# Performance work log

Measured on AMD Instinct MI355X. Metric: run time of the kernel, lower is better.

The kernel has to match this reference:

```python
import jax, jax.numpy as jnp
import numpy as np

N_NODES = 65536
N_EDGES = 524288
N_GRAPHS = 512
G_NODES = 10000
NUM_DISEASES = 2000
IN_DIM = 128
HID = 256  # 2 * IN_DIM (z_emb concat feat)
D_FEAT = 512
C_FEAT = 512
MAX_Z = 4000


def setup_inputs() -> dict:
    key = jax.random.key(0)
    ks = jax.random.split(key, 20)
    rn = lambda k, shape: jax.random.normal(k, shape, dtype=jnp.float32) * 0.05
    return {
        "z": jax.random.randint(ks[0], (N_NODES,), 0, MAX_Z),
        "node_id": jnp.sort(jax.random.randint(ks[1], (N_NODES,), 0, G_NODES)),
        "src": jax.random.randint(ks[2], (N_EDGES,), 0, N_NODES),
        "dst": jax.random.randint(ks[3], (N_EDGES,), 0, N_NODES),
        "graph_ids": jnp.sort(jax.random.randint(ks[4], (N_NODES,), 0, N_GRAPHS)),
        "z_table": rn(ks[5], (MAX_Z, IN_DIM)),
        "d_feat_tab": rn(ks[6], (G_NODES, D_FEAT)),
        "c_feat_tab": rn(ks[7], (G_NODES, C_FEAT)),
        "Wd": rn(ks[8], (D_FEAT, IN_DIM)),
        "Wc": rn(ks[9], (C_FEAT, IN_DIM)),
        "gin_W1": rn(ks[10], (HID, HID)), "gin_b1": jnp.zeros((HID,), jnp.float32),
        "gin_W2": rn(ks[11], (HID, HID)), "gin_b2": jnp.zeros((HID,), jnp.float32),
        "sage_Wself": rn(ks[12], (HID, HID)),
        "sage_Wneigh": rn(ks[13], (HID, HID)),
        "sage_b": jnp.zeros((HID,), jnp.float32),
        "lin1_W": rn(ks[14], (HID, HID)), "lin1_b": jnp.zeros((HID,), jnp.float32),
        "lin2_W": rn(ks[15], (HID, 1)), "lin2_b": jnp.zeros((1,), jnp.float32),
    }


def reference(z, node_id, src, dst, graph_ids, z_table, d_feat_tab, c_feat_tab,
              Wd, Wc, gin_W1, gin_b1, gin_W2, gin_b2,
              sage_Wself, sage_Wneigh, sage_b, lin1_W, lin1_b, lin2_W, lin2_b):
    # --- input feature construction (Model.forward) ---
    z_emb = z_table[z]                               # [N, IN_DIM]
    d_proj = d_feat_tab[node_id] @ Wd                # d_fc (bias=False)
    c_proj = c_feat_tab[node_id] @ Wc                # c_fc (bias=False)
    disease = (node_id <= NUM_DISEASES)[:, None]
    # node_id is sorted -> masked concat order == node order
    feat = jnp.where(disease, d_proj, c_proj)        # [N, IN_DIM]
    x = jnp.concatenate([z_emb, feat], axis=1)       # [N, HID]
    # --- GINConv: sum aggregation, eps=0, mlp = Lin->ReLU->Lin ---
    agg = jax.ops.segment_sum(x[src], dst, num_segments=N_NODES)
    h = x + agg
    h = jax.nn.relu(h @ gin_W1 + gin_b1) @ gin_W2 + gin_b2
    # --- SAGEConv('mean'): fc_self(h) + fc_neigh(mean_neighbors) + bias ---
    deg = jax.ops.segment_sum(jnp.ones((N_EDGES,), h.dtype), dst, num_segments=N_NODES)
    mean_n = jax.ops.segment_sum(h[src], dst, num_segments=N_NODES) / jnp.maximum(deg, 1.0)[:, None]
    h = h @ sage_Wself + mean_n @ sage_Wneigh + sage_b
    # --- per-graph max pooling readout ---
    g = jax.ops.segment_max(h, graph_ids, num_segments=N_GRAPHS, indices_are_sorted=True)
    g = jnp.where(jnp.isfinite(g), g, 0.0)           # guard empty graphs
    # --- head: Linear -> ReLU -> (dropout p=0, eval) -> Linear ---
    h = jax.nn.relu(g @ lin1_W + lin1_b)
    return h @ lin2_W + lin2_b                       # [N_GRAPHS, 1]
```

## Files before the change

### kernel.cpp

```cpp
#include <hip/hip_runtime.h>
#include <hip/hip_bf16.h>

#define N_NODES     65536
#define N_EDGES     524288
#define N_GRAPHS    512
#define G_NODES_N   10000
#define NUM_DIS     2000
#define IN_DIM      128
#define HID         256
#define D_FEAT      512
#define POOL_SPLIT  8

typedef _Float16 half8 __attribute__((ext_vector_type(8)));
typedef _Float16 half4v __attribute__((ext_vector_type(4)));
typedef float    f32x4 __attribute__((ext_vector_type(4)));

typedef __attribute__((address_space(1))) const void as1_void;
typedef __attribute__((address_space(3))) void       as3_void;

__global__ __launch_bounds__(256) void wcvt_all_kernel(
    const float* __restrict__ Ws, const float* __restrict__ Wn,
    const float* __restrict__ Wd, const float* __restrict__ Wc,
    _Float16* __restrict__ WsT, _Float16* __restrict__ WnT,
    _Float16* __restrict__ WdT, _Float16* __restrict__ WcT)
{
    __shared__ float tile[64][65];
    const int b = blockIdx.x;
    const float* W; _Float16* T; int K, N, k0, n0;
    if (b < 32) {
        const int mat = b >> 4, t = b & 15;
        K = HID; N = HID; k0 = (t >> 2) * 64; n0 = (t & 3) * 64;
        W = (mat == 0) ? Ws : Wn;
        T = (mat == 0) ? WsT : WnT;
    } else {
        const int bb = b - 32;
        const int mat = bb >> 4, t = bb & 15;
        K = D_FEAT; N = IN_DIM; k0 = (t >> 1) * 64; n0 = (t & 1) * 64;
        W = (mat == 0) ? Wd : Wc;
        T = (mat == 0) ? WdT : WcT;
    }
    const int tx = threadIdx.x & 63, ty = threadIdx.x >> 6;
    #pragma unroll
    for (int r = 0; r < 64; r += 4)
        tile[r + ty][tx] = W[(size_t)(k0 + r + ty) * N + n0 + tx];
    __syncthreads();
    #pragma unroll
    for (int c = 0; c < 64; c += 4)
        T[(size_t)(n0 + c + ty) * K + k0 + tx] = (_Float16)tile[tx][c + ty];
}

__global__ __launch_bounds__(256) void wprep_kernel(
    const float* __restrict__ W1, const float* __restrict__ W2,
    _Float16* __restrict__ W12P)
{
    const int b = blockIdx.x;
    const int mat = b >> 8;
    const int k = b & 255;
    const int n = threadIdx.x;
    const float* W = mat ? W2 : W1;
    const float v = W[(size_t)k * HID + n];
    const size_t idx = (size_t)(mat * 8 + (k >> 5)) * 8192
                     + (size_t)((((k >> 3) & 3) * 256 + n) * 8 + (k & 7));
    W12P[idx] = (_Float16)v;
}

__global__ __launch_bounds__(256) void proj_mfma_kernel(
    const float* __restrict__ dtab, const float* __restrict__ ctab,
    const _Float16* __restrict__ WdT, const _Float16* __restrict__ WcT,
    _Float16* __restrict__ proj)
{
    __shared__ _Float16 Alds[128 * 40];
    __shared__ _Float16 Blds[128 * 40];
    const int blk = blockIdx.x;
    const float* tab; const _Float16* WT; int base, M, bm;
    if (blk < 16) { tab = dtab; WT = WdT; base = 0;           M = NUM_DIS + 1;             bm = blk * 128; }
    else          { tab = ctab; WT = WcT; base = NUM_DIS + 1; M = G_NODES_N - NUM_DIS - 1; bm = (blk - 16) * 128; }
    const int tid  = threadIdx.x;
    const int wave = tid >> 6, lane = tid & 63;
    const int q    = lane >> 4, l16 = lane & 15;
    const int mbase = (wave & 1) * 64, nbase = (wave >> 1) * 64;
    const int r = tid >> 1, s = tid & 1;

    f32x4 acc[4][4] = {};

    for (int kc = 0; kc < 16; ++kc) {
        const int k0 = kc * 32;
        const int arow = min(bm + r, M - 1);
        const float* gA = tab + (size_t)(base + arow) * D_FEAT + k0 + s * 16;
        const _Float16* gB = WT + (size_t)r * D_FEAT + k0 + s * 16;
        const float4 f0 = ((const float4*)gA)[0];
        const float4 f1 = ((const float4*)gA)[1];
        const float4 f2 = ((const float4*)gA)[2];
        const float4 f3 = ((const float4*)gA)[3];
        const half8 hb0 = *(const half8*)gB;
        const half8 hb1 = *(const half8*)(gB + 8);
        half8 h0, h1;
        h0[0]=(_Float16)f0.x; h0[1]=(_Float16)f0.y; h0[2]=(_Float16)f0.z; h0[3]=(_Float16)f0.w;
        h0[4]=(_Float16)f1.x; h0[5]=(_Float16)f1.y; h0[6]=(_Float16)f1.z; h0[7]=(_Float16)f1.w;
        h1[0]=(_Float16)f2.x; h1[1]=(_Float16)f2.y; h1[2]=(_Float16)f2.z; h1[3]=(_Float16)f2.w;
        h1[4]=(_Float16)f3.x; h1[5]=(_Float16)f3.y; h1[6]=(_Float16)f3.z; h1[7]=(_Float16)f3.w;
        __syncthreads();
        *(half8*)&Alds[r * 40 + s * 16]     = h0;
        *(half8*)&Alds[r * 40 + s * 16 + 8] = h1;
        *(half8*)&Blds[r * 40 + s * 16]     = hb0;
        *(half8*)&Blds[r * 40 + s * 16 + 8] = hb1;
        __syncthreads();
        half8 a[4], b[4];
        #pragma unroll
        for (int i = 0; i < 4; ++i)
            a[i] = *(const half8*)&Alds[(mbase + i * 16 + l16) * 40 + q * 8];
        #pragma unroll
        for (int j = 0; j < 4; ++j)
            b[j] = *(const half8*)&Blds[(nbase + j * 16 + l16) * 40 + q * 8];
        #pragma unroll
        for (int i = 0; i < 4; ++i)
            #pragma unroll
            for (int j = 0; j < 4; ++j)
                acc[i][j] = __builtin_amdgcn_mfma_f32_16x16x32_f16(a[i], b[j], acc[i][j], 0, 0, 0);
    }

    #pragma unroll
    for (int j = 0; j < 4; ++j) {
        const int colg = nbase + j * 16 + l16;
        #pragma unroll
        for (int i = 0; i < 4; ++i) {
            #pragma unroll
            for (int rr = 0; rr < 4; ++rr) {
                const int row = bm + mbase + i * 16 + q * 4 + rr;
                if (row < M)
                    proj[(size_t)(base + row) * IN_DIM + colg] = (_Float16)acc[i][j][rr];
            }
        }
    }
}

__global__ __launch_bounds__(256) void hist_kernel(
    const int* __restrict__ dst, int* __restrict__ cnt)
{
    const int e = blockIdx.x * 256 + threadIdx.x;
    if (e < N_EDGES) atomicAdd(&cnt[dst[e]], 1);
}

__global__ __launch_bounds__(256) void seg_sum_kernel(
    const int* __restrict__ cnt, int* __restrict__ seg)
{
    __shared__ int red[256];
    const int t = threadIdx.x;
    const int4 c = *(const int4*)(cnt + blockIdx.x * 1024 + t * 4);
    red[t] = c.x + c.y + c.z + c.w;
    __syncthreads();
    for (int s = 128; s > 0; s >>= 1) {
        if (t < s) red[t] += red[t + s];
        __syncthreads();
    }
    if (t == 0) seg[blockIdx.x] = red[0];
}

__global__ __launch_bounds__(64) void seg_scan_kernel(
    const int* __restrict__ seg, int* __restrict__ segoff,
    int* __restrict__ total_out)
{
    __shared__ int a[64], b[64];
    const int t = threadIdx.x;
    const int v = seg[t];
    a[t] = v;
    __syncthreads();
    int* in = a; int* out = b;
    for (int off = 1; off < 64; off <<= 1) {
        out[t] = in[t] + ((t >= off) ? in[t - off] : 0);
        __syncthreads();
        int* tmp = in; in = out; out = tmp;
    }
    segoff[t] = in[t] - v;
    if (t == 63) total_out[0] = in[63];
}

__global__ __launch_bounds__(256) void local_scan_kernel(
    const int* __restrict__ cnt, const int* __restrict__ segoff,
    int* __restrict__ row_ptr, int* __restrict__ fill)
{
    __shared__ int a[256], b[256];
    const int t = threadIdx.x;
    const int base = blockIdx.x * 1024 + t * 4;
    const int4 c = *(const int4*)(cnt + base);
    const int s = c.x + c.y + c.z + c.w;
    a[t] = s;
    __syncthreads();
    int* in = a; int* out = b;
    for (int off = 1; off < 256; off <<= 1) {
        out[t] = in[t] + ((t >= off) ? in[t - off] : 0);
        __syncthreads();
        int* tmp = in; in = out; out = tmp;
    }
    const int run = in[t] - s + segoff[blockIdx.x];
    int4 r;
    r.x = run; r.y = run + c.x; r.z = r.y + c.y; r.w = r.z + c.z;
    *(int4*)(row_ptr + base) = r;
    *(int4*)(fill + base) = r;
}

__global__ __launch_bounds__(256) void scatter_kernel(
    const int* __restrict__ src, const int* __restrict__ dst,
    int* __restrict__ fill, int* __restrict__ col)
{
    const int e = blockIdx.x * 256 + threadIdx.x;
    if (e < N_EDGES) {
        const int pos = atomicAdd(&fill[dst[e]], 1);
        col[pos] = src[e];
    }
}

__global__ __launch_bounds__(256) void gin_fused_kernel(
    const int* __restrict__ row_ptr, const int* __restrict__ colv,
    const int* __restrict__ z, const int* __restrict__ node_id,
    const float* __restrict__ z_table, const _Float16* __restrict__ proj,
    const _Float16* __restrict__ W12P,
    const float* __restrict__ b1, const float* __restrict__ b2,
    _Float16* __restrict__ H)
{
    __shared__ _Float16 Apanel[32 * 264];
    __shared__ _Float16 Blds[2][8192];

    const int bm   = blockIdx.x * 32;
    const int tid  = threadIdx.x;
    const int wave = tid >> 6, lane = tid & 63;
    const int q    = lane >> 4, l16 = lane & 15;
    const int nbase = wave * 64;

    auto stage = [&](int c, int buf) {
        const _Float16* src = W12P + (size_t)c * 8192;
        #pragma unroll
        for (int tt = 0; tt < 4; ++tt) {
            const int seg = (wave * 4 + tt) * 64 + lane;
            __builtin_amdgcn_global_load_lds((as1_void*)(src + seg * 8),
                (as3_void*)&Blds[buf][(wave * 4 + tt) * 64 * 8], 16, 0, 0);
        }
    };

    stage(0, 0);

    {
        const int r = tid >> 3, p = tid & 7;
        const int gr = bm + r;
        const int beg = row_ptr[gr], end = row_ptr[gr + 1];
        float za[16], pa[16];
        {
            const int zv = z[gr], nv = node_id[gr];
            const float4* zp = (const float4*)(z_table + (size_t)zv * IN_DIM + p * 16);
            const half8*  pp = (const half8*) (proj    + (size_t)nv * IN_DIM + p * 16);
            #pragma unroll
            for (int u = 0; u < 4; ++u) {
                const float4 v = zp[u];
                za[u*4+0]=v.x; za[u*4+1]=v.y; za[u*4+2]=v.z; za[u*4+3]=v.w;
            }
            #pragma unroll
            for (int u = 0; u < 2; ++u) {
                const half8 v = pp[u];
                #pragma unroll
                for (int i = 0; i < 8; ++i) pa[u*8+i] = (float)v[i];
            }
        }
        for (int e = beg; e < end; ++e) {
            const int s = colv[e];
            const int zv = z[s], nv = node_id[s];
            const float4* zp = (const float4*)(z_table + (size_t)zv * IN_DIM + p * 16);
            const half8*  pp = (const half8*) (proj    + (size_t)nv * IN_DIM + p * 16);
            #pragma unroll
            for (int u = 0; u < 4; ++u) {
                const float4 v = zp[u];
                za[u*4+0]+=v.x; za[u*4+1]+=v.y; za[u*4+2]+=v.z; za[u*4+3]+=v.w;
            }
            #pragma unroll
            for (int u = 0; u < 2; ++u) {
                const half8 v = pp[u];
                #pragma unroll
                for (int i = 0; i < 8; ++i) pa[u*8+i] += (float)v[i];
            }
        }
        half8 oz0, oz1, op0, op1;
        #pragma unroll
        for (int i = 0; i < 8; ++i) {
            oz0[i] = (_Float16)za[i];     oz1[i] = (_Float16)za[8 + i];
            op0[i] = (_Float16)pa[i];     op1[i] = (_Float16)pa[8 + i];
        }
        *(half8*)&Apanel[r * 264 + p * 16]           = oz0;
        *(half8*)&Apanel[r * 264 + p * 16 + 8]       = oz1;
        *(half8*)&Apanel[r * 264 + 128 + p * 16]     = op0;
        *(half8*)&Apanel[r * 264 + 128 + p * 16 + 8] = op1;
    }
    __syncthreads();

    f32x4 acc[2][4] = {};
    int pb = 0;
    for (int c = 0; c < 16; ++c) {
        if (c + 1 < 16) stage(c + 1, pb ^ 1);
        if (c == 8) {
            #pragma unroll
            for (int j = 0; j < 4; ++j) {
                const int colg = nbase + j * 16 + l16;
                const float bv = b1[colg];
                #pragma unroll
                for (int i = 0; i < 2; ++i)
                    #pragma unroll
                    for (int rr = 0; rr < 4; ++rr) {
                        const float v = fmaxf(acc[i][j][rr] + bv, 0.0f);
                        Apanel[(i * 16 + q * 4 + rr) * 264 + colg] = (_Float16)v;
                        acc[i][j][rr] = 0.0f;
                    }
            }
            __syncthreads();
        }
        const int kl = (c & 7) * 32;
        half8 a[2], b[4];
        #pragma unroll
        for (int i = 0; i < 2; ++i)
            a[i] = *(const half8*)&Apanel[(i * 16 + l16) * 264 + kl + q * 8];
        #pragma unroll
        for (int j = 0; j < 4; ++j)
            b[j] = *(const half8*)&Blds[pb][(q * 256 + nbase + j * 16 + l16) * 8];
        #pragma unroll
        for (int i = 0; i < 2; ++i)
            #pragma unroll
            for (int j = 0; j < 4; ++j)
                acc[i][j] = __builtin_amdgcn_mfma_f32_16x16x32_f16(a[i], b[j], acc[i][j], 0, 0, 0);
        __syncthreads();
        pb ^= 1;
    }

    #pragma unroll
    for (int j = 0; j < 4; ++j) {
        const int colg = nbase + j * 16 + l16;
        const float bv = b2[colg];
        #pragma unroll
        for (int i = 0; i < 2; ++i)
            #pragma unroll
            for (int rr = 0; rr < 4; ++rr) {
                const int rowg = bm + i * 16 + q * 4 + rr;
                H[(size_t)rowg * HID + colg] = (_Float16)(acc[i][j][rr] + bv);
            }
    }
}

__global__ __launch_bounds__(256) void csr_agg_kernel(
    const int* __restrict__ row_ptr, const int* __restrict__ col,
    const _Float16* __restrict__ F, _Float16* __restrict__ OUT)
{
    const int t = blockIdx.x * 256 + threadIdx.x;
    const int d = t >> 5;
    const int q = t & 31;
    const int beg = row_ptr[d];
    const int end = row_ptr[d + 1];
    float acc[8] = {0.f,0.f,0.f,0.f,0.f,0.f,0.f,0.f};
    int e = beg;
    for (; e + 4 <= end; e += 4) {
        const int s0 = col[e],     s1 = col[e + 1];
        const int s2 = col[e + 2], s3 = col[e + 3];
        const half8 v0 = *(const half8*)(F + (size_t)s0 * HID + q * 8);
        const half8 v1 = *(const half8*)(F + (size_t)s1 * HID + q * 8);
        const half8 v2 = *(const half8*)(F + (size_t)s2 * HID + q * 8);
        const half8 v3 = *(const half8*)(F + (size_t)s3 * HID + q * 8);
        #pragma unroll
        for (int i = 0; i < 8; ++i)
            acc[i] += ((float)v0[i] + (float)v1[i]) + ((float)v2[i] + (float)v3[i]);
    }
    for (; e < end; ++e) {
        const half8 v0 = *(const half8*)(F + (size_t)col[e] * HID + q * 8);
        #pragma unroll
        for (int i = 0; i < 8; ++i) acc[i] += (float)v0[i];
    }
    const float rs = 1.0f / fmaxf((float)(end - beg), 1.0f);
    half8 o;
    #pragma unroll
    for (int i = 0; i < 8; ++i) o[i] = (_Float16)(acc[i] * rs);
    *(half8*)(OUT + (size_t)d * HID + q * 8) = o;
}

__global__ __launch_bounds__(256) void mfma_gemm_kernel(
    const _Float16* __restrict__ A1, const _Float16* __restrict__ A2,
    const _Float16* __restrict__ B1T, const _Float16* __restrict__ B2T,
    const float* __restrict__ bias, _Float16* __restrict__ Ch)
{
    __shared__ _Float16 Alds[128 * 32];
    __shared__ _Float16 Blds[128 * 32];
    const int bm   = blockIdx.x * 128;
    const int bn   = blockIdx.y * 128;
    const int tid  = threadIdx.x;
    const int wave = tid >> 6, lane = tid & 63;
    const int q    = lane >> 4, l16 = lane & 15;
    const int mbase = (wave & 1) * 64, nbase = (wave >> 1) * 64;

    f32x4 acc[4][4] = {};

    for (int kc = 0; kc < 16; ++kc) {
        const int k0 = (kc & 7) * 32;
        const _Float16* Abase = (kc < 8) ? A1 : A2;
        const _Float16* Bbase = (kc < 8) ? B1T : B2T;
        __syncthreads();
        #pragma unroll
        for (int t = 0; t < 2; ++t) {
            const int i   = wave * 128 + t * 64 + lane;
            const int row = i >> 2, s = i & 3;
            const _Float16* gA = Abase + (size_t)(bm + row) * HID + k0 + s * 8;
            const _Float16* gB = Bbase + (size_t)(bn + row) * HID + k0 + s * 8;
            __builtin_amdgcn_global_load_lds(
                (as1_void*)gA, (as3_void*)&Alds[(wave * 128 + t * 64) * 8], 16, 0, 0);
            __builtin_amdgcn_global_load_lds(
                (as1_void*)gB, (as3_void*)&Blds[(wave * 128 + t * 64) * 8], 16, 0, 0);
        }
        __syncthreads();
        half8 a[4], b[4];
        #pragma unroll
        for (int i = 0; i < 4; ++i)
            a[i] = *(const half8*)&Alds[(mbase + i * 16 + l16) * 32 + q * 8];
        #pragma unroll
        for (int j = 0; j < 4; ++j)
            b[j] = *(const half8*)&Blds[(nbase + j * 16 + l16) * 32 + q * 8];
        #pragma unroll
        for (int i = 0; i < 4; ++i)
            #pragma unroll
            for (int j = 0; j < 4; ++j)
                acc[i][j] = __builtin_amdgcn_mfma_f32_16x16x32_f16(a[i], b[j], acc[i][j], 0, 0, 0);
    }

    #pragma unroll
    for (int j = 0; j < 4; ++j) {
        const int colg = bn + nbase + j * 16 + l16;
        const float bv = bias[colg];
        #pragma unroll
        for (int i = 0; i < 4; ++i) {
            #pragma unroll
            for (int rr = 0; rr < 4; ++rr) {
                const int rowg = bm + mbase + i * 16 + q * 4 + rr;
                Ch[(size_t)rowg * HID + colg] = (_Float16)(acc[i][j][rr] + bv);
            }
        }
    }
}

__global__ __launch_bounds__(256) void pool_part_kernel(
    const _Float16* __restrict__ H2, const int* __restrict__ gid,
    float* __restrict__ Gpart)
{
    const int g = blockIdx.y;
    const int sp = blockIdx.x;
    const int j = threadIdx.x;
    int lo = 0, hi = N_NODES;
    while (lo < hi) { const int mid = (lo + hi) >> 1; if (gid[mid] < g) lo = mid + 1; else hi = mid; }
    const int start = lo;
    hi = N_NODES;
    while (lo < hi) { const int mid = (lo + hi) >> 1; if (gid[mid] < g + 1) lo = mid + 1; else hi = mid; }
    const int end = lo;
    float m = -INFINITY;
    for (int i = start + sp; i < end; i += POOL_SPLIT)
        m = fmaxf(m, (float)H2[(size_t)i * HID + j]);
    Gpart[((size_t)g * POOL_SPLIT + sp) * HID + j] = m;
}

__global__ __launch_bounds__(256) void head_kernel(
    const float* __restrict__ Gpart,
    const float* __restrict__ W1, const float* __restrict__ b1,
    const float* __restrict__ W2, const float* __restrict__ b2,
    float* __restrict__ out)
{
    const int g = blockIdx.x;
    const int j = threadIdx.x;
    __shared__ float row[HID];
    __shared__ float red[HID];
    float m = -INFINITY;
    #pragma unroll
    for (int sp = 0; sp < POOL_SPLIT; ++sp)
        m = fmaxf(m, Gpart[((size_t)g * POOL_SPLIT + sp) * HID + j]);
    row[j] = (m == -INFINITY) ? 0.0f : m;
    __syncthreads();
    float acc = b1[j];
    #pragma unroll 8
    for (int k = 0; k < HID; ++k)
        acc = fmaf(row[k], W1[k * HID + j], acc);
    acc = fmaxf(acc, 0.f);
    red[j] = acc * W2[j];
    __syncthreads();
    for (int s = 128; s > 0; s >>= 1) {
        if (j < s) red[j] += red[j + s];
        __syncthreads();
    }
    if (j == 0) out[g] = red[0] + b2[0];
}

extern "C" void kernel_launch(void* const* d_in, const int* in_sizes, int n_in,
                              void* d_out, int out_size, void* d_ws, size_t ws_size,
                              hipStream_t stream)
{
    const int*   z         = (const int*)d_in[0];
    const int*   node_id   = (const int*)d_in[1];
    const int*   src       = (const int*)d_in[2];
    const int*   dst       = (const int*)d_in[3];
    const int*   graph_ids = (const int*)d_in[4];
    const float* z_table   = (const float*)d_in[5];
    const float* d_feat    = (const float*)d_in[6];
    const float* c_feat    = (const float*)d_in[7];
    const float* Wd        = (const float*)d_in[8];
    const float* Wc        = (const float*)d_in[9];
    const float* gin_W1    = (const float*)d_in[10];
    const float* gin_b1    = (const float*)d_in[11];
    const float* gin_W2    = (const float*)d_in[12];
    const float* gin_b2    = (const float*)d_in[13];
    const float* sage_Wself  = (const float*)d_in[14];
    const float* sage_Wneigh = (const float*)d_in[15];
    const float* sage_b    = (const float*)d_in[16];
    const float* lin1_W    = (const float*)d_in[17];
    const float* lin1_b    = (const float*)d_in[18];
    const float* lin2_W    = (const float*)d_in[19];
    const float* lin2_b    = (const float*)d_in[20];
    float* out = (float*)d_out;

    const size_t NH = (size_t)N_NODES * HID;
    char* wsb = (char*)d_ws;
    _Float16* Hh   = (_Float16*)wsb;                     wsb += NH * 2;
    _Float16* AGGh = (_Float16*)wsb;                     wsb += NH * 2;
    _Float16* H2h  = (_Float16*)wsb;                     wsb += NH * 2;
    _Float16* projh= (_Float16*)wsb;                     wsb += (size_t)G_NODES_N * IN_DIM * 2;
    _Float16* W12P = (_Float16*)wsb;                     wsb += 16 * 8192 * 2;
    _Float16* WsT  = (_Float16*)wsb;                     wsb += HID * HID * 2;
    _Float16* WnT  = (_Float16*)wsb;                     wsb += HID * HID * 2;
    _Float16* WdT  = (_Float16*)wsb;                     wsb += D_FEAT * IN_DIM * 2;
    _Float16* WcT  = (_Float16*)wsb;                     wsb += D_FEAT * IN_DIM * 2;
    float* Gpart   = (float*)wsb;                        wsb += (size_t)N_GRAPHS * POOL_SPLIT * HID * 4;
    int* row_ptr   = (int*)wsb;                          wsb += (N_NODES + 4) * 4;
    int* cnt       = (int*)wsb;                          wsb += N_NODES * 4;
    int* fill      = (int*)wsb;                          wsb += N_NODES * 4;
    int* col       = (int*)wsb;                          wsb += N_EDGES * 4;
    int* seg       = (int*)wsb;                          wsb += 64 * 4;
    int* segoff    = (int*)wsb;                          wsb += 64 * 4;

    hipMemsetAsync(cnt, 0, N_NODES * sizeof(int), stream);
    hist_kernel<<<N_EDGES / 256, 256, 0, stream>>>(dst, cnt);
    seg_sum_kernel<<<64, 256, 0, stream>>>(cnt, seg);
    seg_scan_kernel<<<1, 64, 0, stream>>>(seg, segoff, &row_ptr[N_NODES]);
    local_scan_kernel<<<64, 256, 0, stream>>>(cnt, segoff, row_ptr, fill);
    scatter_kernel<<<N_EDGES / 256, 256, 0, stream>>>(src, dst, fill, col);

    wcvt_all_kernel<<<64, 256, 0, stream>>>(sage_Wself, sage_Wneigh, Wd, Wc,
                                            WsT, WnT, WdT, WcT);
    wprep_kernel<<<512, 256, 0, stream>>>(gin_W1, gin_W2, W12P);

    proj_mfma_kernel<<<16 + 63, 256, 0, stream>>>(d_feat, c_feat, WdT, WcT, projh);

    gin_fused_kernel<<<N_NODES / 32, 256, 0, stream>>>(
        row_ptr, col, z, node_id, z_table, projh, W12P, gin_b1, gin_b2, Hh);

    csr_agg_kernel<<<(N_NODES * 32) / 256, 256, 0, stream>>>(row_ptr, col, Hh, AGGh);

    dim3 ggrid(N_NODES / 128, HID / 128);
    mfma_gemm_kernel<<<ggrid, 256, 0, stream>>>(Hh, AGGh, WsT, WnT, sage_b, H2h);

    dim3 pgrid(POOL_SPLIT, N_GRAPHS);
    pool_part_kernel<<<pgrid, 256, 0, stream>>>(H2h, graph_ids, Gpart);
    head_kernel<<<N_GRAPHS, 256, 0, stream>>>(Gpart, lin1_W, lin1_b, lin2_W, lin2_b, out);
}
```

Baseline: 390.3 us.

## Merge prep kernels, fuse scan with decoupled lookback, use fp16 z-table gather

Folds the weight transposes, W1/W2 packing, z_table fp16 conversion, cnt zeroing and z/node_id interleaving into one prep kernel, replacing a memset and two launches. The three-kernel CSR scan becomes a single kernel that chains block prefixes through spin-waiting flags. The GIN gather reads a packed int2 (z,node_id) and an fp16 z table, halving embedding bytes per neighbour and removing one dependent load. This cuts launch count and gather traffic, but the spin-wait depends on all 64 scan blocks being co-resident, and the fp16 z table adds rounding.

```diff
diff --git a/kernel.cpp b/kernel.cpp
--- a/kernel.cpp
+++ b/kernel.cpp
@@ -9,59 +9,77 @@
 #define IN_DIM      128
 #define HID         256
 #define D_FEAT      512
+#define MAX_Z       4000
 #define POOL_SPLIT  8
 
 typedef _Float16 half8 __attribute__((ext_vector_type(8)));
-typedef _Float16 half4v __attribute__((ext_vector_type(4)));
 typedef float    f32x4 __attribute__((ext_vector_type(4)));
 
 typedef __attribute__((address_space(1))) const void as1_void;
 typedef __attribute__((address_space(3))) void       as3_void;
 
-__global__ __launch_bounds__(256) void wcvt_all_kernel(
+__global__ __launch_bounds__(256) void prep_kernel(
     const float* __restrict__ Ws, const float* __restrict__ Wn,
     const float* __restrict__ Wd, const float* __restrict__ Wc,
+    const float* __restrict__ W1, const float* __restrict__ W2,
+    const float* __restrict__ z_table,
+    const int* __restrict__ z, const int* __restrict__ node_id,
     _Float16* __restrict__ WsT, _Float16* __restrict__ WnT,
-    _Float16* __restrict__ WdT, _Float16* __restrict__ WcT)
-{
-    __shared__ float tile[64][65];
+    _Float16* __restrict__ WdT, _Float16* __restrict__ WcT,
+    _Float16* __restrict__ W12P, _Float16* __restrict__ zt16,
+    int2* __restrict__ zn2, int* __restrict__ cnt, int* __restrict__ flags)
+{
     const int b = blockIdx.x;
-    const float* W; _Float16* T; int K, N, k0, n0;
-    if (b < 32) {
-        const int mat = b >> 4, t = b & 15;
-        K = HID; N = HID; k0 = (t >> 2) * 64; n0 = (t & 3) * 64;
-        W = (mat == 0) ? Ws : Wn;
-        T = (mat == 0) ? WsT : WnT;
+    const int tid = threadIdx.x;
+    if (b < 64) {
+        __shared__ float tile[64][65];
+        const float* W; _Float16* T; int K, N, k0, n0;
+        if (b < 32) {
+            const int mat = b >> 4, t = b & 15;
+            K = HID; N = HID; k0 = (t >> 2) * 64; n0 = (t & 3) * 64;
+            W = (mat == 0) ? Ws : Wn;
+            T = (mat == 0) ? WsT : WnT;
+        } else {
+            const int bb = b - 32;
+            const int mat = bb >> 4, t = bb & 15;
+            K = D_FEAT; N = IN_DIM; k0 = (t >> 1) * 64; n0 = (t & 1) * 64;
+            W = (mat == 0) ? Wd : Wc;
+            T = (mat == 0) ? WdT : WcT;
+        }
+        const int tx = tid & 63, ty = tid >> 6;
+        #pragma unroll
+        for (int r = 0; r < 64; r += 4)
+            tile[r + ty][tx] = W[(size_t)(k0 + r + ty) * N + n0 + tx];
+        __syncthreads();
+        #pragma unroll
+        for (int c = 0; c < 64; c += 4)
+            T[(size_t)(n0 + c + ty) * K + k0 + tx] = (_Float16)tile[tx][c + ty];
+    } else if (b < 576) {
+        const int bb = b - 64;
+        const int mat = bb >> 8;
+        const int k = bb & 255;
+        const int n = tid;
+        const float* W = mat ? W2 : W1;
+        const float v = W[(size_t)k * HID + n];
+        const size_t idx = (size_t)(mat * 8 + (k >> 5)) * 8192
+                         + (size_t)((((k >> 3) & 3) * 256 + n) * 8 + (k & 7));
+        W12P[idx] = (_Float16)v;
+    } else if (b < 826) {
+        const size_t base = ((size_t)(b - 576) * 256 + tid) * 8;
+        const float4 f0 = *(const float4*)(z_table + base);
+        const float4 f1 = *(const float4*)(z_table + base + 4);
+        half8 h;
+        h[0]=(_Float16)f0.x; h[1]=(_Float16)f0.y; h[2]=(_Float16)f0.z; h[3]=(_Float16)f0.w;
+        h[4]=(_Float16)f1.x; h[5]=(_Float16)f1.y; h[6]=(_Float16)f1.z; h[7]=(_Float16)f1.w;
+        *(half8*)(zt16 + base) = h;
+    } else if (b < 890) {
+        const int base = (b - 826) * 1024 + tid * 4;
+        *(int4*)(cnt + base) = make_int4(0, 0, 0, 0);
+        if (b == 826 && tid < 128) flags[tid] = 0;
     } else {
-        const int bb = b - 32;
-        const int mat = bb >> 4, t = bb & 15;
-        K = D_FEAT; N = IN_DIM; k0 = (t >> 1) * 64; n0 = (t & 1) * 64;
-        W = (mat == 0) ? Wd : Wc;
-        T = (mat == 0) ? WdT : WcT;
-    }
-    const int tx = threadIdx.x & 63, ty = threadIdx.x >> 6;
-    #pragma unroll
-    for (int r = 0; r < 64; r += 4)
-        tile[r + ty][tx] = W[(size_t)(k0 + r + ty) * N + n0 + tx];
-    __syncthreads();
-    #pragma unroll
-    for (int c = 0; c < 64; c += 4)
-        T[(size_t)(n0 + c + ty) * K + k0 + tx] = (_Float16)tile[tx][c + ty];
-}
-
-__global__ __launch_bounds__(256) void wprep_kernel(
-    const float* __restrict__ W1, const float* __restrict__ W2,
-    _Float16* __restrict__ W12P)
-{
-    const int b = blockIdx.x;
-    const int mat = b >> 8;
-    const int k = b & 255;
-    const int n = threadIdx.x;
-    const float* W = mat ? W2 : W1;
-    const float v = W[(size_t)k * HID + n];
-    const size_t idx = (size_t)(mat * 8 + (k >> 5)) * 8192
-                     + (size_t)((((k >> 3) & 3) * 256 + n) * 8 + (k & 7));
-    W12P[idx] = (_Float16)v;
+        const int i = (b - 890) * 256 + tid;
+        zn2[i] = make_int2(z[i], node_id[i]);
+    }
 }
 
 __global__ __launch_bounds__(256) void proj_mfma_kernel(
@@ -141,47 +159,15 @@
     if (e < N_EDGES) atomicAdd(&cnt[dst[e]], 1);
 }
 
-__global__ __launch_bounds__(256) void seg_sum_kernel(
-    const int* __restrict__ cnt, int* __restrict__ seg)
-{
-    __shared__ int red[256];
+__global__ __launch_bounds__(256) void scan_fused_kernel(
+    const int* __restrict__ cnt, int* __restrict__ row_ptr,
+    int* __restrict__ fill, int* __restrict__ flags)
+{
+    __shared__ int a[256], b[256];
+    __shared__ int segbase;
     const int t = threadIdx.x;
-    const int4 c = *(const int4*)(cnt + blockIdx.x * 1024 + t * 4);
-    red[t] = c.x + c.y + c.z + c.w;
-    __syncthreads();
-    for (int s = 128; s > 0; s >>= 1) {
-        if (t < s) red[t] += red[t + s];
-        __syncthreads();
-    }
-    if (t == 0) seg[blockIdx.x] = red[0];
-}
-
-__global__ __launch_bounds__(64) void seg_scan_kernel(
-    const int* __restrict__ seg, int* __restrict__ segoff,
-    int* __restrict__ total_out)
-{
-    __shared__ int a[64], b[64];
-    const int t = threadIdx.x;
-    const int v = seg[t];
-    a[t] = v;
-    __syncthreads();
-    int* in = a; int* out = b;
-    for (int off = 1; off < 64; off <<= 1) {
-        out[t] = in[t] + ((t >= off) ? in[t - off] : 0);
-        __syncthreads();
-        int* tmp = in; in = out; out = tmp;
-    }
-    segoff[t] = in[t] - v;
-    if (t == 63) total_out[0] = in[63];
-}
-
-__global__ __launch_bounds__(256) void local_scan_kernel(
-    const int* __restrict__ cnt, const int* __restrict__ segoff,
-    int* __restrict__ row_ptr, int* __restrict__ fill)
-{
-    __shared__ int a[256], b[256];
-    const int t = threadIdx.x;
-    const int base = blockIdx.x * 1024 + t * 4;
+    const int blk = blockIdx.x;
+    const int base = blk * 1024 + t * 4;
     const int4 c = *(const int4*)(cnt + base);
     const int s = c.x + c.y + c.z + c.w;
     a[t] = s;
@@ -192,7 +178,21 @@
         __syncthreads();
         int* tmp = in; in = out; out = tmp;
     }
-    const int run = in[t] - s + segoff[blockIdx.x];
+    if (t == 255) {
+        const int blocksum = in[255];
+        int pfx = 0;
+        if (blk > 0) {
+            while (atomicAdd(&flags[blk - 1], 0) == 0) {}
+            pfx = atomicAdd(&flags[64 + blk - 1], 0);
+        }
+        atomicExch(&flags[64 + blk], pfx + blocksum);
+        __threadfence();
+        atomicExch(&flags[blk], 1);
+        segbase = pfx;
+        if (blk == 63) row_ptr[N_NODES] = pfx + blocksum;
+    }
+    __syncthreads();
+    const int run = in[t] - s + segbase;
     int4 r;
     r.x = run; r.y = run + c.x; r.z = r.y + c.y; r.w = r.z + c.z;
     *(int4*)(row_ptr + base) = r;
@@ -212,8 +212,8 @@
 
 __global__ __launch_bounds__(256) void gin_fused_kernel(
     const int* __restrict__ row_ptr, const int* __restrict__ colv,
-    const int* __restrict__ z, const int* __restrict__ node_id,
-    const float* __restrict__ z_table, const _Float16* __restrict__ proj,
+    const int2* __restrict__ zn2,
+    const _Float16* __restrict__ zt16, const _Float16* __restrict__ proj,
     const _Float16* __restrict__ W12P,
     const float* __restrict__ b1, const float* __restrict__ b2,
     _Float16* __restrict__ H)
@@ -245,36 +245,25 @@
         const int beg = row_ptr[gr], end = row_ptr[gr + 1];
         float za[16], pa[16];
         {
-            const int zv = z[gr], nv = node_id[gr];
-            const float4* zp = (const float4*)(z_table + (size_t)zv * IN_DIM + p * 16);
-            const half8*  pp = (const half8*) (proj    + (size_t)nv * IN_DIM + p * 16);
-            #pragma unroll
-            for (int u = 0; u < 4; ++u) {
-                const float4 v = zp[u];
-                za[u*4+0]=v.x; za[u*4+1]=v.y; za[u*4+2]=v.z; za[u*4+3]=v.w;
+            const int2 zn = zn2[gr];
+            const half8* zp = (const half8*)(zt16 + (size_t)zn.x * IN_DIM + p * 16);
+            const half8* pp = (const half8*)(proj + (size_t)zn.y * IN_DIM + p * 16);
+            const half8 z0 = zp[0], z1 = zp[1], p0 = pp[0], p1 = pp[1];
+            #pragma unroll
+            for (int i = 0; i < 8; ++i) {
+                za[i] = (float)z0[i]; za[8 + i] = (float)z1[i];
+                pa[i] = (float)p0[i]; pa[8 + i] = (float)p1[i];
             }
-            #pragma unroll
-            for (int u = 0; u < 2; ++u) {
-                const half8 v = pp[u];
-                #pragma unroll
-                for (int i = 0; i < 8; ++i) pa[u*8+i] = (float)v[i];
-            }
         }
         for (int e = beg; e < end; ++e) {
-            const int s = colv[e];
-            const int zv = z[s], nv = node_id[s];
-            const float4* zp = (const float4*)(z_table + (size_t)zv * IN_DIM + p * 16);
-            const half8*  pp = (const half8*) (proj    + (size_t)nv * IN_DIM + p * 16);
-            #pragma unroll
-            for (int u = 0; u < 4; ++u) {
-                const float4 v = zp[u];
-                za[u*4+0]+=v.x; za[u*4+1]+=v.y; za[u*4+2]+=v.z; za[u*4+3]+=v.w;
-            }
-            #pragma unroll
-            for (int u = 0; u < 2; ++u) {
-                const half8 v = pp[u];
-                #pragma unroll
-                for (int i = 0; i < 8; ++i) pa[u*8+i] += (float)v[i];
+            const int2 zn = zn2[colv[e]];
+            const half8* zp = (const half8*)(zt16 + (size_t)zn.x * IN_DIM + p * 16);
+            const half8* pp = (const half8*)(proj + (size_t)zn.y * IN_DIM + p * 16);
+            const half8 z0 = zp[0], z1 = zp[1], p0 = pp[0], p1 = pp[1];
+            #pragma unroll
+            for (int i = 0; i < 8; ++i) {
+                za[i] += (float)z0[i]; za[8 + i] += (float)z1[i];
+                pa[i] += (float)p0[i]; pa[8 + i] += (float)p1[i];
             }
         }
         half8 oz0, oz1, op0, op1;
@@ -524,29 +513,27 @@
     _Float16* WnT  = (_Float16*)wsb;                     wsb += HID * HID * 2;
     _Float16* WdT  = (_Float16*)wsb;                     wsb += D_FEAT * IN_DIM * 2;
     _Float16* WcT  = (_Float16*)wsb;                     wsb += D_FEAT * IN_DIM * 2;
+    _Float16* zt16 = (_Float16*)wsb;                     wsb += (size_t)MAX_Z * IN_DIM * 2;
+    int2* zn2      = (int2*)wsb;                         wsb += (size_t)N_NODES * 8;
     float* Gpart   = (float*)wsb;                        wsb += (size_t)N_GRAPHS * POOL_SPLIT * HID * 4;
     int* row_ptr   = (int*)wsb;                          wsb += (N_NODES + 4) * 4;
     int* cnt       = (int*)wsb;                          wsb += N_NODES * 4;
     int* fill      = (int*)wsb;                          wsb += N_NODES * 4;
     int* col       = (int*)wsb;                          wsb += N_EDGES * 4;
-    int* seg       = (int*)wsb;                          wsb += 64 * 4;
-    int* segoff    = (int*)wsb;                          wsb += 64 * 4;
-
-    hipMemsetAsync(cnt, 0, N_NODES * sizeof(int), stream);
+    int* flags     = (int*)wsb;                          wsb += 128 * 4;
+
+    prep_kernel<<<1146, 256, 0, stream>>>(
+        sage_Wself, sage_Wneigh, Wd, Wc, gin_W1, gin_W2, z_table, z, node_id,
+        WsT, WnT, WdT, WcT, W12P, zt16, zn2, cnt, flags);
+
     hist_kernel<<<N_EDGES / 256, 256, 0, stream>>>(dst, cnt);
-    seg_sum_kernel<<<64, 256, 0, stream>>>(cnt, seg);
-    seg_scan_kernel<<<1, 64, 0, stream>>>(seg, segoff, &row_ptr[N_NODES]);
-    local_scan_kernel<<<64, 256, 0, stream>>>(cnt, segoff, row_ptr, fill);
+    scan_fused_kernel<<<64, 256, 0, stream>>>(cnt, row_ptr, fill, flags);
     scatter_kernel<<<N_EDGES / 256, 256, 0, stream>>>(src, dst, fill, col);
 
-    wcvt_all_kernel<<<64, 256, 0, stream>>>(sage_Wself, sage_Wneigh, Wd, Wc,
-                                            WsT, WnT, WdT, WcT);
-    wprep_kernel<<<512, 256, 0, stream>>>(gin_W1, gin_W2, W12P);
-
     proj_mfma_kernel<<<16 + 63, 256, 0, stream>>>(d_feat, c_feat, WdT, WcT, projh);
 
     gin_fused_kernel<<<N_NODES / 32, 256, 0, stream>>>(
-        row_ptr, col, z, node_id, z_table, projh, W12P, gin_b1, gin_b2, Hh);
+        row_ptr, col, zn2, zt16, projh, W12P, gin_b1, gin_b2, Hh);
 
     csr_agg_kernel<<<(N_NODES * 32) / 256, 256, 0, stream>>>(row_ptr, col, Hh, AGGh);
 
```

Result: slower. 447.2 us (+14.6%).
